# Kernel tuning notes

Hardware: AMD Instinct MI355X
Metric: run time of the kernel (lower is better)

The kernel has to match this reference:

```python
import jax, jax.numpy as jnp
import numpy as np

WIN = 25            # window size (win_h == win_w == 25)
DIM = 256           # channels
DIM_HEAD = 32
HEADS = DIM // DIM_HEAD   # 8
HIDDEN = int(DIM * 2.0)   # mlp_ratio = 2.0
EPS = 1e-5


def _rel_pos_indices(w=WIN):
    # replicates the buffer built in Attention.__init__
    pos = np.arange(w)
    gi, gj = np.meshgrid(pos, pos, indexing='ij')
    grid = np.stack([gi.ravel(), gj.ravel()], axis=-1)          # (w*w, 2)
    rel = grid[:, None, :] - grid[None, :, :] + (w - 1)          # (n, n, 2)
    return jnp.asarray(rel[..., 0] * (2 * w - 1) + rel[..., 1])  # (n, n) int


def setup_inputs() -> dict:
    key = jax.random.key(0)
    ks = jax.random.split(key, 8)
    s = 0.02
    d = DIM
    return {
        'x': jax.random.normal(ks[0], (2, d, 100, 100), jnp.float32),
        'w_qkv': jax.random.normal(ks[1], (3 * d, d), jnp.float32) * s,
        'w_out': jax.random.normal(ks[2], (d, d), jnp.float32) * s,
        'rel_bias_table': jax.random.normal(ks[3], ((2 * WIN - 1) ** 2, HEADS), jnp.float32) * s,
        'gamma2': jnp.ones((d,), jnp.float32),
        'beta2': jnp.zeros((d,), jnp.float32),
        'w1': jax.random.normal(ks[4], (HIDDEN, d), jnp.float32) * s,
        'b1': jnp.zeros((HIDDEN,), jnp.float32),
        'w2': jax.random.normal(ks[5], (d, HIDDEN), jnp.float32) * s,
        'b2': jnp.zeros((d,), jnp.float32),
    }


def _layernorm(x, g, b, eps=EPS):
    m = x.mean(-1, keepdims=True)
    v = ((x - m) ** 2).mean(-1, keepdims=True)
    return (x - m) / jnp.sqrt(v + eps) * g + b


def reference(x, w_qkv, w_out, rel_bias_table, gamma2, beta2, w1, b1, w2, b2):
    b, d, H, W = x.shape
    nh, nw = H // WIN, W // WIN
    h, dh = HEADS, DIM_HEAD
    scale = dh ** -0.5
    n = WIN * WIN

    # --- window partition: (b, d, H, W) -> (b*nh*nw, n, d) ---
    xw = x.reshape(b, d, nh, WIN, nw, WIN).transpose(0, 2, 4, 3, 5, 1)
    xw = xw.reshape(b * nh * nw, n, d)

    # --- windowed attention with relative-position bias (norm1 unused in source) ---
    qkv = xw @ w_qkv.T                         # (B, n, 3d)
    q, k, v = jnp.split(qkv, 3, axis=-1)
    split_heads = lambda t: t.reshape(t.shape[0], n, h, dh).transpose(0, 2, 1, 3)
    q = split_heads(q) * scale                 # (B, h, n, dh)
    k = split_heads(k)
    v = split_heads(v)

    sim = jnp.einsum('bhid,bhjd->bhij', q, k)  # (B, h, n, n)
    bias = rel_bias_table[_rel_pos_indices()]  # (n, n, h)
    sim = sim + bias.transpose(2, 0, 1)[None]
    attn = jax.nn.softmax(sim, axis=-1)
    out = jnp.einsum('bhij,bhjd->bhid', attn, v)            # (B, h, n, dh)
    out = out.transpose(0, 2, 1, 3).reshape(-1, n, d)        # head-major concat: (m d)
    out = out @ w_out.T                                      # (B, n, d)

    # --- un-partition: (b*nh*nw, n, d) -> (b, d, H, W) ---
    xa = out.reshape(b, nh, nw, WIN, WIN, d).transpose(0, 5, 1, 3, 2, 4)
    xa = xa.reshape(b, d, H, W)

    # --- norm2 + MLP + residual ---
    y = xa.transpose(0, 2, 3, 1).reshape(b, H * W, d)
    y = _layernorm(y, gamma2, beta2)
    y = jax.nn.gelu(y @ w1.T + b1, approximate=False) @ w2.T + b2
    y = y.reshape(b, H, W, d).transpose(0, 3, 1, 2)
    return x + y
```

## Files before the change

kernel.cpp:

```cpp
#include <hip/hip_runtime.h>


using f32x4 = __attribute__((ext_vector_type(4))) float;
using s16x8 = __attribute__((ext_vector_type(8))) short;
using u32x4 = __attribute__((ext_vector_type(4))) unsigned;

__device__ __forceinline__ ushort f2b(float f) {
  union { float f; unsigned u; } v; v.f = f;
  return (ushort)((v.u + 0x7FFFu + ((v.u >> 16) & 1u)) >> 16);
}
__device__ __forceinline__ ushort f2b_fast(float f) {
  union { float f; unsigned u; } v; v.f = f;
  return (ushort)((v.u + 0x8000u) >> 16);
}
__device__ __forceinline__ float b2f(ushort u) {
  union { unsigned u; float f; } v; v.u = ((unsigned)u) << 16; return v.f;
}
__device__ __forceinline__ float lo2f(unsigned w) {
  union { unsigned u; float f; } v; v.u = w << 16; return v.f;
}
__device__ __forceinline__ float hi2f(unsigned w) {
  union { unsigned u; float f; } v; v.u = w & 0xffff0000u; return v.f;
}

__device__ __forceinline__ unsigned cvtpk(float lo, float hi) {
  unsigned r;
  asm("v_cvt_pk_bf16_f32 %0, %1, %2" : "=v"(r) : "v"(lo), "v"(hi));
  return r;
}
__device__ __forceinline__ void pl32(unsigned& a, unsigned& b) {
  asm("v_permlane32_swap_b32 %0, %1" : "+v"(a), "+v"(b));
}
__device__ __forceinline__ void pl16(unsigned& a, unsigned& b) {
  asm("v_permlane16_swap_b32 %0, %1" : "+v"(a), "+v"(b));
}

__device__ __forceinline__ void gld16(const void* g, void* l) {
  __builtin_amdgcn_global_load_lds((const __attribute__((address_space(1))) void*)g,
                                   (__attribute__((address_space(3))) void*)l, 16, 0, 0);
}

template<int KB>
__device__ __forceinline__ void gemm_core(const ushort* __restrict__ A, int lda,
                                          const ushort* __restrict__ B, int ldb,
                                          f32x4 acc[4][4]) {
  __shared__ ushort As[128 * 64];
  __shared__ ushort Bs[128 * 64];
  const int tid = threadIdx.x;
  const int lane = tid & 63;
  const int wv = tid >> 6;
  const int wr = (wv >> 1) * 64;
  const int wc = (wv & 1) * 64;
  const int srow = (lane >> 3);
  const int sg = ((lane & 7) ^ (srow & 7)) * 8;
  f32x4 zero = {0.f, 0.f, 0.f, 0.f};
#pragma unroll
  for (int mt = 0; mt < 4; ++mt)
#pragma unroll
    for (int nt = 0; nt < 4; ++nt) acc[mt][nt] = zero;

  for (int kb = 0; kb < KB; ++kb) {
#pragma unroll
    for (int j = 0; j < 4; ++j) {
      int r0 = wv * 32 + j * 8;
      int row = r0 + srow;
      gld16(A + row * lda + kb * 64 + sg, &As[r0 * 64]);
      gld16(B + row * ldb + kb * 64 + sg, &Bs[r0 * 64]);
    }
    __syncthreads();
#pragma unroll
    for (int ks = 0; ks < 2; ++ks) {
      s16x8 af[4], bfr[4];
      const int G = ks * 4 + (lane >> 4);
#pragma unroll
      for (int mt = 0; mt < 4; ++mt) {
        int row = wr + mt * 16 + (lane & 15);
        af[mt] = *(const s16x8*)&As[row * 64 + (G ^ (row & 7)) * 8];
      }
#pragma unroll
      for (int nt = 0; nt < 4; ++nt) {
        int row = wc + nt * 16 + (lane & 15);
        bfr[nt] = *(const s16x8*)&Bs[row * 64 + (G ^ (row & 7)) * 8];
      }
#pragma unroll
      for (int mt = 0; mt < 4; ++mt)
#pragma unroll
        for (int nt = 0; nt < 4; ++nt)
          acc[mt][nt] = __builtin_amdgcn_mfma_f32_16x16x32_bf16(af[mt], bfr[nt], acc[mt][nt], 0, 0, 0);
    }
    __syncthreads();
  }
}

__global__ __launch_bounds__(256) void k_prep(const float* __restrict__ x,
                                              const float* __restrict__ wqkv,
                                              const float* __restrict__ wout,
                                              const float* __restrict__ w1,
                                              const float* __restrict__ w2,
                                              const float* __restrict__ table,
                                              ushort* __restrict__ Xw,
                                              ushort* __restrict__ wqkvb,
                                              ushort* __restrict__ woutb,
                                              ushort* __restrict__ w1b,
                                              ushort* __restrict__ w2b,
                                              ushort* __restrict__ biasPh) {
  __shared__ ushort smem[64 * 264];
  const int bid = blockIdx.x, tid = threadIdx.x;
  if (bid < 320) {
    ushort (*Ls)[264] = (ushort(*)[264])smem;
    const int t0 = bid * 64;
    const int w = t0 / 640;
    const int tokbase = t0 - w * 640;
    const int b = w >> 4, wh = (w >> 2) & 3, ww = w & 3;
    for (int i = tid; i < 64 * 256; i += 256) {
      int c = i >> 6, tl = i & 63;
      int tok = tokbase + tl;
      ushort val = 0;
      if (tok < 625) {
        int ii = tok / 25, jj = tok - ii * 25;
        val = f2b(x[((b * 256 + c) * 100 + wh * 25 + ii) * 100 + ww * 25 + jj]);
      }
      Ls[tl][c] = val;
    }
    __syncthreads();
    for (int i = tid; i < 64 * 32; i += 256) {
      int tl = i >> 5, g = (i & 31) * 8;
      *(uint4*)(Xw + (t0 + tl) * 256 + g) = *(const uint4*)&Ls[tl][g];
    }
  } else if (bid < 832) {
    int v = (bid - 320) * 1024 + tid * 4;
    const float* src; ushort* dst; int off;
    if (v < 196608)      { src = wqkv; dst = wqkvb; off = v; }
    else if (v < 262144) { src = wout; dst = woutb; off = v - 196608; }
    else if (v < 393216) { src = w1;   dst = w1b;   off = v - 262144; }
    else                 { src = w2;   dst = w2b;   off = v - 393216; }
    float4 f = *(const float4*)(src + off);
    ushort4 u; u.x = f2b(f.x); u.y = f2b(f.y); u.z = f2b(f.z); u.w = f2b(f.w);
    *(ushort4*)(dst + off) = u;
  } else {
    float* tl = (float*)smem;
    const int qb = bid - 832;
    const int h = qb / 40, t = qb - (qb / 40) * 40;
    for (int i = tid; i < 2401; i += 256) tl[i] = table[i * 8 + h] * 1.4426950408889634f;
    __syncthreads();
    const int lane = tid >> 2, rr = tid & 3;
    const int quad = lane >> 4, cl = lane & 15;
    int qrow = t * 16 + cl;
    int qg = (qrow < 625) ? qrow : 0;
    const int ri = qg / 25, ci = qg - ri * 25;
    for (int cc = 0; cc < 4; ++cc)
      for (int cp = 0; cp < 5; ++cp)
#pragma unroll
        for (int codd = 0; codd < 2; ++codd) {
          int kv = cc * 160 + (cp * 2 + codd) * 16 + quad * 4 + rr;
          float v = -1e30f;
          if (kv < 625) {
            int rj = kv / 25, cj = kv - rj * 25;
            v = tl[(ri - rj + 24) * 49 + (ci - cj + 24)];
          }
          biasPh[((((h * 40 + t) * 4 + cc) * 5 + cp) * 64 + lane) * 8 + codd * 4 + rr] = f2b(v);
        }
  }
}

__global__ __launch_bounds__(256) void k_qkv(const ushort* __restrict__ Xw,
                                             const ushort* __restrict__ Wb,
                                             ushort* __restrict__ Qb,
                                             ushort* __restrict__ Kb,
                                             ushort* __restrict__ VbT) {
  f32x4 acc[4][4];
  gemm_core<4>(Xw + blockIdx.x * 128 * 256, 256, Wb + blockIdx.y * 128 * 256, 256, acc);
  const int lane = threadIdx.x & 63, wv = threadIdx.x >> 6;
  const int wr = (wv >> 1) * 64, wc = (wv & 1) * 64;
  const int which = blockIdx.y >> 1;
  const float QSC = 0.17677669529663687f * 1.4426950408889634f;
#pragma unroll
  for (int mt = 0; mt < 4; ++mt) {
#pragma unroll
    for (int nt = 0; nt < 4; ++nt) {
      int n = blockIdx.y * 128 + wc + nt * 16 + (lane & 15);
      int h = (n >> 5) & 7, ch = n & 31;
      int m0 = blockIdx.x * 128 + wr + mt * 16 + (lane >> 4) * 4;
      int w = m0 / 640, tok0 = m0 - w * 640;
      if (which == 2) {
        ushort4 pk;
        pk.x = f2b_fast(acc[mt][nt][0]); pk.y = f2b_fast(acc[mt][nt][1]);
        pk.z = f2b_fast(acc[mt][nt][2]); pk.w = f2b_fast(acc[mt][nt][3]);
        *(ushort4*)(VbT + (((w << 3) + h) * 32 + ch) * 640 + tok0) = pk;
      } else {
        ushort* dst = which == 0 ? Qb : Kb;
        float sc = which == 0 ? QSC : 1.f;
#pragma unroll
        for (int r = 0; r < 4; ++r)
          dst[(((w << 3) + h) * 640 + tok0 + r) * 32 + ch] = f2b_fast(acc[mt][nt][r] * sc);
      }
    }
  }
}

__global__ __launch_bounds__(128, 3) void k_attn(const ushort* __restrict__ Qb,
                                                 const ushort* __restrict__ Kb,
                                                 const ushort* __restrict__ VbT,
                                                 const ushort* __restrict__ biasPh,
                                                 ushort* __restrict__ AO) {
  const int tid = threadIdx.x;
  const int lane = tid & 63;
  const int wv = tid >> 6;
  const int quad = lane >> 4;
  const int cl = lane & 15;
  const int bid = blockIdx.x;
  const int h = bid & 7;
  const int rem = bid >> 3;
  const int win = rem / 5;
  const int tg = rem - win * 5;
  const ushort* Qg = Qb + (win * 8 + h) * 20480;
  const ushort* Kg = Kb + (win * 8 + h) * 20480;
  const ushort* Vt = VbT + (win * 8 + h) * 20480;

  const int t0 = tg * 8 + wv * 4;
  s16x8 qf[4];
#pragma unroll
  for (int tlp = 0; tlp < 4; ++tlp)
    qf[tlp] = *(const s16x8*)(Qg + ((t0 + tlp) * 16 + cl) * 32 + quad * 8);

  const f32x4 zero = {0.f, 0.f, 0.f, 0.f};
  f32x4 o0[4], o1[4];
  float ssum[4];
#pragma unroll
  for (int tlp = 0; tlp < 4; ++tlp) { o0[tlp] = zero; o1[tlp] = zero; ssum[tlp] = 0.f; }

  const ushort* bpB = biasPh + ((h * 40 + t0) * 20) * 512 + lane * 8;

  for (int ch2 = 0; ch2 < 10; ++ch2) {
    s16x8 kf[4], va[2], vb[2];
#pragma unroll
    for (int j = 0; j < 4; ++j)
      kf[j] = *(const s16x8*)(Kg + (ch2 * 64 + j * 16 + cl) * 32 + quad * 8);
#pragma unroll
    for (int j = 0; j < 2; ++j) {
      va[j] = *(const s16x8*)(Vt + cl * 640 + ch2 * 64 + j * 32 + quad * 8);
      vb[j] = *(const s16x8*)(Vt + (16 + cl) * 640 + ch2 * 64 + j * 32 + quad * 8);
    }
    __builtin_amdgcn_sched_barrier(0);
#pragma unroll
    for (int tlp = 0; tlp < 4; ++tlp) {
      const s16x8 bb0 = *(const s16x8*)(bpB + (tlp * 20 + 2 * ch2) * 512);
      const s16x8 bb1 = *(const s16x8*)(bpB + (tlp * 20 + 2 * ch2 + 1) * 512);
      const unsigned* w0 = (const unsigned*)&bb0;
      const unsigned* w1 = (const unsigned*)&bb1;
      f32x4 s0, s1, s2, s3;
      s0[0] = lo2f(w0[0]); s0[1] = hi2f(w0[0]); s0[2] = lo2f(w0[1]); s0[3] = hi2f(w0[1]);
      s1[0] = lo2f(w0[2]); s1[1] = hi2f(w0[2]); s1[2] = lo2f(w0[3]); s1[3] = hi2f(w0[3]);
      s2[0] = lo2f(w1[0]); s2[1] = hi2f(w1[0]); s2[2] = lo2f(w1[1]); s2[3] = hi2f(w1[1]);
      s3[0] = lo2f(w1[2]); s3[1] = hi2f(w1[2]); s3[2] = lo2f(w1[3]); s3[3] = hi2f(w1[3]);
      s0 = __builtin_amdgcn_mfma_f32_16x16x32_bf16(kf[0], qf[tlp], s0, 0, 0, 0);
      s1 = __builtin_amdgcn_mfma_f32_16x16x32_bf16(kf[1], qf[tlp], s1, 0, 0, 0);
      s2 = __builtin_amdgcn_mfma_f32_16x16x32_bf16(kf[2], qf[tlp], s2, 0, 0, 0);
      s3 = __builtin_amdgcn_mfma_f32_16x16x32_bf16(kf[3], qf[tlp], s3, 0, 0, 0);
#pragma unroll
      for (int r = 0; r < 4; ++r) {
        s0[r] = __builtin_amdgcn_exp2f(s0[r]);
        s1[r] = __builtin_amdgcn_exp2f(s1[r]);
        s2[r] = __builtin_amdgcn_exp2f(s2[r]);
        s3[r] = __builtin_amdgcn_exp2f(s3[r]);
      }
      ssum[tlp] += ((s0[0] + s0[1]) + (s0[2] + s0[3])) + ((s1[0] + s1[1]) + (s1[2] + s1[3]))
                 + ((s2[0] + s2[1]) + (s2[2] + s2[3])) + ((s3[0] + s3[1]) + (s3[2] + s3[3]));
      unsigned a0 = cvtpk(s0[0], s0[1]);
      unsigned a1 = cvtpk(s0[2], s0[3]);
      unsigned b0 = cvtpk(s1[0], s1[1]);
      unsigned b1 = cvtpk(s1[2], s1[3]);
      pl32(a0, b0); pl16(a0, b0);
      pl32(a1, b1); pl16(a1, b1);
      u32x4 pw0; pw0[0] = a0; pw0[1] = a1; pw0[2] = b0; pw0[3] = b1;
      s16x8 pf0 = __builtin_bit_cast(s16x8, pw0);
      o0[tlp] = __builtin_amdgcn_mfma_f32_16x16x32_bf16(va[0], pf0, o0[tlp], 0, 0, 0);
      o1[tlp] = __builtin_amdgcn_mfma_f32_16x16x32_bf16(vb[0], pf0, o1[tlp], 0, 0, 0);
      unsigned a2 = cvtpk(s2[0], s2[1]);
      unsigned a3 = cvtpk(s2[2], s2[3]);
      unsigned b2 = cvtpk(s3[0], s3[1]);
      unsigned b3 = cvtpk(s3[2], s3[3]);
      pl32(a2, b2); pl16(a2, b2);
      pl32(a3, b3); pl16(a3, b3);
      u32x4 pw1; pw1[0] = a2; pw1[1] = a3; pw1[2] = b2; pw1[3] = b3;
      s16x8 pf1 = __builtin_bit_cast(s16x8, pw1);
      o0[tlp] = __builtin_amdgcn_mfma_f32_16x16x32_bf16(va[1], pf1, o0[tlp], 0, 0, 0);
      o1[tlp] = __builtin_amdgcn_mfma_f32_16x16x32_bf16(vb[1], pf1, o1[tlp], 0, 0, 0);
    }
  }
#pragma unroll
  for (int tlp = 0; tlp < 4; ++tlp) {
    float s = ssum[tlp];
    unsigned ua = __builtin_bit_cast(unsigned, s), ub = ua;
    pl32(ua, ub);
    s = __builtin_bit_cast(float, ua) + __builtin_bit_cast(float, ub);
    ua = __builtin_bit_cast(unsigned, s); ub = ua;
    pl16(ua, ub);
    s = __builtin_bit_cast(float, ua) + __builtin_bit_cast(float, ub);
    int tok = (t0 + tlp) * 16 + cl;
    if (tok < 625) {
      float inv = 1.f / s;
      int base = (win * 640 + tok) * 256 + h * 32 + quad * 4;
      ushort4 p0, p1;
      p0.x = f2b_fast(o0[tlp][0] * inv); p0.y = f2b_fast(o0[tlp][1] * inv);
      p0.z = f2b_fast(o0[tlp][2] * inv); p0.w = f2b_fast(o0[tlp][3] * inv);
      p1.x = f2b_fast(o1[tlp][0] * inv); p1.y = f2b_fast(o1[tlp][1] * inv);
      p1.z = f2b_fast(o1[tlp][2] * inv); p1.w = f2b_fast(o1[tlp][3] * inv);
      *(ushort4*)(AO + base) = p0;
      *(ushort4*)(AO + base + 16) = p1;
    }
  }
}

__global__ __launch_bounds__(256, 2) void k_out_ln(const ushort* __restrict__ AO,
                                                   const ushort* __restrict__ Wb,
                                                   const float* __restrict__ gamma,
                                                   const float* __restrict__ beta,
                                                   ushort* __restrict__ Yn) {
  __shared__ ushort As[64 * 64];
  __shared__ ushort Bs[256 * 64];
  __shared__ float red[2][64][2];
  const int tid = threadIdx.x;
  const int lane = tid & 63;
  const int wv = tid >> 6;
  const int wr = (wv >> 1) * 32, wc = (wv & 1) * 128;
  const int quad = lane >> 4, cl = lane & 15;
  const int srow = lane >> 3;
  const int sg = ((lane & 7) ^ (srow & 7)) * 8;
  f32x4 zero = {0.f, 0.f, 0.f, 0.f};
  f32x4 acc[2][8];
#pragma unroll
  for (int mt = 0; mt < 2; ++mt)
#pragma unroll
    for (int nt = 0; nt < 8; ++nt) acc[mt][nt] = zero;

  const ushort* A = AO + blockIdx.x * 64 * 256;
  for (int kb = 0; kb < 4; ++kb) {
#pragma unroll
    for (int i = 0; i < 10; ++i) {
      int r0 = (wv + i * 4) * 8;
      int row = r0 + srow;
      if (r0 < 64) gld16(A + row * 256 + kb * 64 + sg, &As[r0 * 64]);
      else         gld16(Wb + (row - 64) * 256 + kb * 64 + sg, &Bs[(r0 - 64) * 64]);
    }
    __syncthreads();
#pragma unroll
    for (int ks = 0; ks < 2; ++ks) {
      s16x8 af[2], bfr[8];
      const int G = ks * 4 + quad;
#pragma unroll
      for (int mt = 0; mt < 2; ++mt) {
        int row = wr + mt * 16 + cl;
        af[mt] = *(const s16x8*)&As[row * 64 + (G ^ (row & 7)) * 8];
      }
#pragma unroll
      for (int nt = 0; nt < 8; ++nt) {
        int row = wc + nt * 16 + cl;
        bfr[nt] = *(const s16x8*)&Bs[row * 64 + (G ^ (row & 7)) * 8];
      }
#pragma unroll
      for (int mt = 0; mt < 2; ++mt)
#pragma unroll
        for (int nt = 0; nt < 8; ++nt)
          acc[mt][nt] = __builtin_amdgcn_mfma_f32_16x16x32_bf16(af[mt], bfr[nt], acc[mt][nt], 0, 0, 0);
    }
    __syncthreads();
  }
#pragma unroll
  for (int mt = 0; mt < 2; ++mt)
#pragma unroll
    for (int r = 0; r < 4; ++r) {
      float s = 0.f, ss = 0.f;
#pragma unroll
      for (int nt = 0; nt < 8; ++nt) { float v = acc[mt][nt][r]; s += v; ss += v * v; }
      s += __shfl_xor(s, 1, 64); ss += __shfl_xor(ss, 1, 64);
      s += __shfl_xor(s, 2, 64); ss += __shfl_xor(ss, 2, 64);
      s += __shfl_xor(s, 4, 64); ss += __shfl_xor(ss, 4, 64);
      s += __shfl_xor(s, 8, 64); ss += __shfl_xor(ss, 8, 64);
      if (cl == 0) {
        int row = wr + mt * 16 + quad * 4 + r;
        red[wc >> 7][row][0] = s;
        red[wc >> 7][row][1] = ss;
      }
    }
  __syncthreads();
  float g[8], bt[8];
#pragma unroll
  for (int nt = 0; nt < 8; ++nt) { int n = wc + nt * 16 + cl; g[nt] = gamma[n]; bt[nt] = beta[n]; }
  const int m0 = blockIdx.x * 64;
#pragma unroll
  for (int mt = 0; mt < 2; ++mt)
#pragma unroll
    for (int r = 0; r < 4; ++r) {
      int row = wr + mt * 16 + quad * 4 + r;
      int m = m0 + row;
      int w = m / 640, tok = m - w * 640;
      if (tok < 625) {
        float sum = red[0][row][0] + red[1][row][0];
        float ssum = red[0][row][1] + red[1][row][1];
        float mean = sum * 0.00390625f;
        float var = ssum * 0.00390625f - mean * mean;
        float rstd = rsqrtf(var + 1e-5f);
        int b = w >> 4, whh = (w >> 2) & 3, www = w & 3;
        int ii = tok / 25, jj = tok - ii * 25;
        int p = (whh * 25 + ii) * 100 + www * 25 + jj;
        ushort* dst = Yn + (b * 10000 + p) * 256;
#pragma unroll
        for (int nt = 0; nt < 8; ++nt) {
          float v = (acc[mt][nt][r] - mean) * rstd * g[nt] + bt[nt];
          dst[wc + nt * 16 + cl] = f2b_fast(v);
        }
      }
    }
}

__global__ __launch_bounds__(256) void k_fc1(const ushort* __restrict__ Yn,
                                             const ushort* __restrict__ W1b,
                                             const float* __restrict__ b1,
                                             ushort* __restrict__ G) {
  f32x4 acc[4][4];
  gemm_core<4>(Yn + blockIdx.x * 128 * 256, 256, W1b + blockIdx.y * 128 * 256, 256, acc);
  const int lane = threadIdx.x & 63, wv = threadIdx.x >> 6;
  const int wr = (wv >> 1) * 64, wc = (wv & 1) * 64;
#pragma unroll
  for (int mt = 0; mt < 4; ++mt)
#pragma unroll
    for (int nt = 0; nt < 4; ++nt) {
      int n = blockIdx.y * 128 + wc + nt * 16 + (lane & 15);
      float bias = b1[n];
#pragma unroll
      for (int r = 0; r < 4; ++r) {
        int m = blockIdx.x * 128 + wr + mt * 16 + (lane >> 4) * 4 + r;
        float v = acc[mt][nt][r] + bias;
        v = 0.5f * v * (1.f + erff(v * 0.70710678118f));
        G[m * 512 + n] = f2b_fast(v);
      }
    }
}

__global__ __launch_bounds__(256) void k_fc2(const ushort* __restrict__ W2b,
                                             const ushort* __restrict__ G,
                                             const float* __restrict__ b2,
                                             const float* __restrict__ x,
                                             float* __restrict__ out) {
  f32x4 acc[4][4];
  gemm_core<8>(W2b + blockIdx.x * 128 * 512, 512, G + blockIdx.y * 128 * 512, 512, acc);
  const int lane = threadIdx.x & 63, wv = threadIdx.x >> 6;
  const int wr = (wv >> 1) * 64, wc = (wv & 1) * 64;
#pragma unroll
  for (int mt = 0; mt < 4; ++mt)
#pragma unroll
    for (int nt = 0; nt < 4; ++nt) {
      int t = blockIdx.y * 128 + wc + nt * 16 + (lane & 15);
      if (t < 20000) {
        int b = t / 10000, p = t - b * 10000;
#pragma unroll
        for (int r = 0; r < 4; ++r) {
          int c = blockIdx.x * 128 + wr + mt * 16 + (lane >> 4) * 4 + r;
          int idx = (b * 256 + c) * 10000 + p;
          out[idx] = x[idx] + acc[mt][nt][r] + b2[c];
        }
      }
    }
}

extern "C" void kernel_launch(void* const* d_in, const int* in_sizes, int n_in,
                              void* d_out, int out_size, void* d_ws, size_t ws_size,
                              hipStream_t stream) {
  const float* x     = (const float*)d_in[0];
  const float* wqkv  = (const float*)d_in[1];
  const float* wout  = (const float*)d_in[2];
  const float* bias  = (const float*)d_in[3];
  const float* gamma = (const float*)d_in[4];
  const float* beta  = (const float*)d_in[5];
  const float* w1    = (const float*)d_in[6];
  const float* b1    = (const float*)d_in[7];
  const float* w2    = (const float*)d_in[8];
  const float* b2    = (const float*)d_in[9];
  float* out = (float*)d_out;
  char* ws = (char*)d_ws;

  ushort* Xw    = (ushort*)(ws + 0);
  ushort* AO    = Xw;
  ushort* wqkvb = (ushort*)(ws + 10485760);
  ushort* woutb = (ushort*)(ws + 10878976);
  ushort* w1b   = (ushort*)(ws + 11010048);
  ushort* w2b   = (ushort*)(ws + 11272192);
  ushort* Qb    = (ushort*)(ws + 11534336);
  ushort* Kb    = (ushort*)(ws + 22020096);
  ushort* VbT   = (ushort*)(ws + 32505856);
  ushort* biasPh= (ushort*)(ws + 42991616);
  ushort* Yn    = (ushort*)(ws + 22020096);
  ushort* G     = (ushort*)(ws + 32505856);

  k_prep  <<<1152, 256, 0, stream>>>(x, wqkv, wout, w1, w2, bias,
                                     Xw, wqkvb, woutb, w1b, w2b, biasPh);
  k_qkv   <<<dim3(160, 6), 256, 0, stream>>>(Xw, wqkvb, Qb, Kb, VbT);
  k_attn  <<<1280, 128, 0, stream>>>(Qb, Kb, VbT, biasPh, AO);
  k_out_ln<<<320, 256, 0, stream>>>(AO, woutb, gamma, beta, Yn);
  k_fc1   <<<dim3(157, 4), 256, 0, stream>>>(Yn, w1b, b1, G);
  k_fc2   <<<dim3(2, 157), 256, 0, stream>>>(w2b, G, b2, x, out);
}
```

Before: 208.4 us.

## Double-buffer activation tiles in LDS, read weights from global, prefetch K/V

```diff
diff --git a/kernel.cpp b/kernel.cpp
--- a/kernel.cpp
+++ b/kernel.cpp
@@ -41,17 +41,17 @@
 }
 
 template<int KB>
-__device__ __forceinline__ void gemm_core(const ushort* __restrict__ A, int lda,
-                                          const ushort* __restrict__ B, int ldb,
-                                          f32x4 acc[4][4]) {
-  __shared__ ushort As[128 * 64];
-  __shared__ ushort Bs[128 * 64];
+__device__ __forceinline__ void gemm_sA(const ushort* __restrict__ A, int lda,
+                                        const ushort* __restrict__ W, int ldw,
+                                        f32x4 acc[4][4]) {
+  __shared__ ushort As[2][128 * 64];
   const int tid = threadIdx.x;
   const int lane = tid & 63;
   const int wv = tid >> 6;
   const int wr = (wv >> 1) * 64;
   const int wc = (wv & 1) * 64;
-  const int srow = (lane >> 3);
+  const int quad = lane >> 4, cl = lane & 15;
+  const int srow = lane >> 3;
   const int sg = ((lane & 7) ^ (srow & 7)) * 8;
   f32x4 zero = {0.f, 0.f, 0.f, 0.f};
 #pragma unroll
@@ -59,28 +59,38 @@
 #pragma unroll
     for (int nt = 0; nt < 4; ++nt) acc[mt][nt] = zero;
 
-  for (int kb = 0; kb < KB; ++kb) {
+  auto STAGE = [&](int kb, int b) {
 #pragma unroll
     for (int j = 0; j < 4; ++j) {
       int r0 = wv * 32 + j * 8;
-      int row = r0 + srow;
-      gld16(A + row * lda + kb * 64 + sg, &As[r0 * 64]);
-      gld16(B + row * ldb + kb * 64 + sg, &Bs[r0 * 64]);
-    }
-    __syncthreads();
+      gld16(A + (r0 + srow) * lda + kb * 64 + sg, &As[b][r0 * 64]);
+    }
+  };
+  STAGE(0, 0);
+#pragma unroll
+  for (int kb = 0; kb < KB; ++kb) {
+    const int cur = kb & 1;
+    if (kb + 1 < KB) {
+      STAGE(kb + 1, cur ^ 1);
+      asm volatile("s_waitcnt vmcnt(4)" ::: "memory");
+    } else {
+      asm volatile("s_waitcnt vmcnt(0)" ::: "memory");
+    }
+    __builtin_amdgcn_s_barrier();
+    __builtin_amdgcn_sched_barrier(0);
 #pragma unroll
     for (int ks = 0; ks < 2; ++ks) {
+      const int G = ks * 4 + quad;
       s16x8 af[4], bfr[4];
-      const int G = ks * 4 + (lane >> 4);
+#pragma unroll
+      for (int nt = 0; nt < 4; ++nt) {
+        int row = wc + nt * 16 + cl;
+        bfr[nt] = *(const s16x8*)(W + row * ldw + kb * 64 + G * 8);
+      }
 #pragma unroll
       for (int mt = 0; mt < 4; ++mt) {
-        int row = wr + mt * 16 + (lane & 15);
-        af[mt] = *(const s16x8*)&As[row * 64 + (G ^ (row & 7)) * 8];
-      }
-#pragma unroll
-      for (int nt = 0; nt < 4; ++nt) {
-        int row = wc + nt * 16 + (lane & 15);
-        bfr[nt] = *(const s16x8*)&Bs[row * 64 + (G ^ (row & 7)) * 8];
+        int row = wr + mt * 16 + cl;
+        af[mt] = *(const s16x8*)&As[cur][row * 64 + (G ^ (row & 7)) * 8];
       }
 #pragma unroll
       for (int mt = 0; mt < 4; ++mt)
@@ -88,7 +98,69 @@
         for (int nt = 0; nt < 4; ++nt)
           acc[mt][nt] = __builtin_amdgcn_mfma_f32_16x16x32_bf16(af[mt], bfr[nt], acc[mt][nt], 0, 0, 0);
     }
-    __syncthreads();
+    if (kb + 1 < KB) __syncthreads();
+  }
+}
+
+template<int KB>
+__device__ __forceinline__ void gemm_sB(const ushort* __restrict__ W, int ldw,
+                                        const ushort* __restrict__ B, int ldb,
+                                        f32x4 acc[4][4]) {
+  __shared__ ushort Bs[2][128 * 64];
+  const int tid = threadIdx.x;
+  const int lane = tid & 63;
+  const int wv = tid >> 6;
+  const int wr = (wv >> 1) * 64;
+  const int wc = (wv & 1) * 64;
+  const int quad = lane >> 4, cl = lane & 15;
+  const int srow = lane >> 3;
+  const int sg = ((lane & 7) ^ (srow & 7)) * 8;
+  f32x4 zero = {0.f, 0.f, 0.f, 0.f};
+#pragma unroll
+  for (int mt = 0; mt < 4; ++mt)
+#pragma unroll
+    for (int nt = 0; nt < 4; ++nt) acc[mt][nt] = zero;
+
+  auto STAGE = [&](int kb, int b) {
+#pragma unroll
+    for (int j = 0; j < 4; ++j) {
+      int r0 = wv * 32 + j * 8;
+      gld16(B + (r0 + srow) * ldb + kb * 64 + sg, &Bs[b][r0 * 64]);
+    }
+  };
+  STAGE(0, 0);
+#pragma unroll
+  for (int kb = 0; kb < KB; ++kb) {
+    const int cur = kb & 1;
+    if (kb + 1 < KB) {
+      STAGE(kb + 1, cur ^ 1);
+      asm volatile("s_waitcnt vmcnt(4)" ::: "memory");
+    } else {
+      asm volatile("s_waitcnt vmcnt(0)" ::: "memory");
+    }
+    __builtin_amdgcn_s_barrier();
+    __builtin_amdgcn_sched_barrier(0);
+#pragma unroll
+    for (int ks = 0; ks < 2; ++ks) {
+      const int G = ks * 4 + quad;
+      s16x8 af[4], bfr[4];
+#pragma unroll
+      for (int mt = 0; mt < 4; ++mt) {
+        int row = wr + mt * 16 + cl;
+        af[mt] = *(const s16x8*)(W + row * ldw + kb * 64 + G * 8);
+      }
+#pragma unroll
+      for (int nt = 0; nt < 4; ++nt) {
+        int row = wc + nt * 16 + cl;
+        bfr[nt] = *(const s16x8*)&Bs[cur][row * 64 + (G ^ (row & 7)) * 8];
+      }
+#pragma unroll
+      for (int mt = 0; mt < 4; ++mt)
+#pragma unroll
+        for (int nt = 0; nt < 4; ++nt)
+          acc[mt][nt] = __builtin_amdgcn_mfma_f32_16x16x32_bf16(af[mt], bfr[nt], acc[mt][nt], 0, 0, 0);
+    }
+    if (kb + 1 < KB) __syncthreads();
   }
 }
 
@@ -169,7 +241,7 @@
                                              ushort* __restrict__ Kb,
                                              ushort* __restrict__ VbT) {
   f32x4 acc[4][4];
-  gemm_core<4>(Xw + blockIdx.x * 128 * 256, 256, Wb + blockIdx.y * 128 * 256, 256, acc);
+  gemm_sA<4>(Xw + blockIdx.x * 128 * 256, 256, Wb + blockIdx.y * 128 * 256, 256, acc);
   const int lane = threadIdx.x & 63, wv = threadIdx.x >> 6;
   const int wr = (wv >> 1) * 64, wc = (wv & 1) * 64;
   const int which = blockIdx.y >> 1;
@@ -231,16 +303,25 @@
 
   const ushort* bpB = biasPh + ((h * 40 + t0) * 20) * 512 + lane * 8;
 
+#define LOADK(c2, KF, VA, VB)                                                        \
+  {                                                                                  \
+    _Pragma("unroll")                                                                \
+    for (int j = 0; j < 4; ++j)                                                      \
+      KF[j] = *(const s16x8*)(Kg + ((c2) * 64 + j * 16 + cl) * 32 + quad * 8);       \
+    _Pragma("unroll")                                                                \
+    for (int j = 0; j < 2; ++j) {                                                    \
+      VA[j] = *(const s16x8*)(Vt + cl * 640 + (c2) * 64 + j * 32 + quad * 8);        \
+      VB[j] = *(const s16x8*)(Vt + (16 + cl) * 640 + (c2) * 64 + j * 32 + quad * 8); \
+    }                                                                                \
+  }
+
+  s16x8 kf[4], va[2], vb[2];
+  s16x8 kn[4], van[2], vbn[2];
+  LOADK(0, kf, va, vb);
+
+#pragma unroll
   for (int ch2 = 0; ch2 < 10; ++ch2) {
-    s16x8 kf[4], va[2], vb[2];
-#pragma unroll
-    for (int j = 0; j < 4; ++j)
-      kf[j] = *(const s16x8*)(Kg + (ch2 * 64 + j * 16 + cl) * 32 + quad * 8);
-#pragma unroll
-    for (int j = 0; j < 2; ++j) {
-      va[j] = *(const s16x8*)(Vt + cl * 640 + ch2 * 64 + j * 32 + quad * 8);
-      vb[j] = *(const s16x8*)(Vt + (16 + cl) * 640 + ch2 * 64 + j * 32 + quad * 8);
-    }
+    if (ch2 < 9) LOADK(ch2 + 1, kn, van, vbn);
     __builtin_amdgcn_sched_barrier(0);
 #pragma unroll
     for (int tlp = 0; tlp < 4; ++tlp) {
@@ -287,7 +368,14 @@
       o0[tlp] = __builtin_amdgcn_mfma_f32_16x16x32_bf16(va[1], pf1, o0[tlp], 0, 0, 0);
       o1[tlp] = __builtin_amdgcn_mfma_f32_16x16x32_bf16(vb[1], pf1, o1[tlp], 0, 0, 0);
     }
-  }
+    __builtin_amdgcn_sched_barrier(0);
+    if (ch2 < 9) {
+#pragma unroll
+      for (int j = 0; j < 4; ++j) kf[j] = kn[j];
+      va[0] = van[0]; va[1] = van[1]; vb[0] = vbn[0]; vb[1] = vbn[1];
+    }
+  }
+#undef LOADK
 #pragma unroll
   for (int tlp = 0; tlp < 4; ++tlp) {
     float s = ssum[tlp];
@@ -317,8 +405,7 @@
                                                    const float* __restrict__ gamma,
                                                    const float* __restrict__ beta,
                                                    ushort* __restrict__ Yn) {
-  __shared__ ushort As[64 * 64];
-  __shared__ ushort Bs[256 * 64];
+  __shared__ ushort As[2][64 * 64];
   __shared__ float red[2][64][2];
   const int tid = threadIdx.x;
   const int lane = tid & 63;
@@ -335,28 +422,38 @@
     for (int nt = 0; nt < 8; ++nt) acc[mt][nt] = zero;
 
   const ushort* A = AO + blockIdx.x * 64 * 256;
+  auto STAGE = [&](int kb, int b) {
+#pragma unroll
+    for (int i = 0; i < 2; ++i) {
+      int r0 = (wv + i * 4) * 8;
+      gld16(A + (r0 + srow) * 256 + kb * 64 + sg, &As[b][r0 * 64]);
+    }
+  };
+  STAGE(0, 0);
+#pragma unroll
   for (int kb = 0; kb < 4; ++kb) {
-#pragma unroll
-    for (int i = 0; i < 10; ++i) {
-      int r0 = (wv + i * 4) * 8;
-      int row = r0 + srow;
-      if (r0 < 64) gld16(A + row * 256 + kb * 64 + sg, &As[r0 * 64]);
-      else         gld16(Wb + (row - 64) * 256 + kb * 64 + sg, &Bs[(r0 - 64) * 64]);
-    }
-    __syncthreads();
+    const int cur = kb & 1;
+    if (kb < 3) {
+      STAGE(kb + 1, cur ^ 1);
+      asm volatile("s_waitcnt vmcnt(2)" ::: "memory");
+    } else {
+      asm volatile("s_waitcnt vmcnt(0)" ::: "memory");
+    }
+    __builtin_amdgcn_s_barrier();
+    __builtin_amdgcn_sched_barrier(0);
 #pragma unroll
     for (int ks = 0; ks < 2; ++ks) {
+      const int G = ks * 4 + quad;
       s16x8 af[2], bfr[8];
-      const int G = ks * 4 + quad;
+#pragma unroll
+      for (int nt = 0; nt < 8; ++nt) {
+        int row = wc + nt * 16 + cl;
+        bfr[nt] = *(const s16x8*)(Wb + row * 256 + kb * 64 + G * 8);
+      }
 #pragma unroll
       for (int mt = 0; mt < 2; ++mt) {
         int row = wr + mt * 16 + cl;
-        af[mt] = *(const s16x8*)&As[row * 64 + (G ^ (row & 7)) * 8];
-      }
-#pragma unroll
-      for (int nt = 0; nt < 8; ++nt) {
-        int row = wc + nt * 16 + cl;
-        bfr[nt] = *(const s16x8*)&Bs[row * 64 + (G ^ (row & 7)) * 8];
+        af[mt] = *(const s16x8*)&As[cur][row * 64 + (G ^ (row & 7)) * 8];
       }
 #pragma unroll
       for (int mt = 0; mt < 2; ++mt)
@@ -364,7 +461,7 @@
         for (int nt = 0; nt < 8; ++nt)
           acc[mt][nt] = __builtin_amdgcn_mfma_f32_16x16x32_bf16(af[mt], bfr[nt], acc[mt][nt], 0, 0, 0);
     }
-    __syncthreads();
+    if (kb < 3) __syncthreads();
   }
 #pragma unroll
   for (int mt = 0; mt < 2; ++mt)
@@ -419,7 +516,7 @@
                                              const float* __restrict__ b1,
                                              ushort* __restrict__ G) {
   f32x4 acc[4][4];
-  gemm_core<4>(Yn + blockIdx.x * 128 * 256, 256, W1b + blockIdx.y * 128 * 256, 256, acc);
+  gemm_sA<4>(Yn + blockIdx.x * 128 * 256, 256, W1b + blockIdx.y * 128 * 256, 256, acc);
   const int lane = threadIdx.x & 63, wv = threadIdx.x >> 6;
   const int wr = (wv >> 1) * 64, wc = (wv & 1) * 64;
 #pragma unroll
@@ -444,7 +541,7 @@
                                              const float* __restrict__ x,
                                              float* __restrict__ out) {
   f32x4 acc[4][4];
-  gemm_core<8>(W2b + blockIdx.x * 128 * 512, 512, G + blockIdx.y * 128 * 512, 512, acc);
+  gemm_sB<8>(W2b + blockIdx.x * 128 * 512, 512, G + blockIdx.y * 128 * 512, 512, acc);
   const int lane = threadIdx.x & 63, wv = threadIdx.x >> 6;
   const int wr = (wv >> 1) * 64, wc = (wv & 1) * 64;
 #pragma unroll
```

Result: slower. 408.7 us (+96.1%).
